# Kernel optimization log

Hardware: AMD Instinct MI355X
Metric: run time of the kernel (lower is better)

The kernel has to match this reference:

```python
import jax, jax.numpy as jnp
import numpy as np

S = 8192  # query length
T = 8192  # key/value length
D = 256   # head dim


def setup_inputs() -> dict:
    key = jax.random.key(0)
    kq, kk, kv = jax.random.split(key, 3)
    return {
        "query": jax.random.normal(kq, (S, D), dtype=jnp.float32),
        "key": jax.random.normal(kk, (T, D), dtype=jnp.float32),
        "value": jax.random.normal(kv, (T, D), dtype=jnp.float32),
    }


def reference(query, key, value):
    # attn_weights = Q @ K^T  (contract last dims, no batch dims)  -> [S, T]
    attn_weights = jnp.einsum("sd,td->st", query, key)
    # SoftmaxAttn: softmax over axes [ndim//2, ndim) == last axis for 2D
    attn_weights = jax.nn.softmax(attn_weights, axis=-1).astype(jnp.float32)
    # y = A @ V  -> [S, D]
    y = jnp.einsum("st,td->sd", attn_weights, value)
    return y
```

## Files before the change

kernel.cpp:

```cpp
#include <hip/hip_runtime.h>
#include <hip/hip_fp16.h>

#define S_LEN 8192
#define T_LEN 8192
#define D_DIM 256
#define QBLK 128
#define KVBLK 32
#define TSPLIT 8
#define NKV ((T_LEN / TSPLIT) / KVBLK)
#define NQT (S_LEN / QBLK)
#define KTILE_BYTES 16384
#define VTILE_BYTES 16384
#define RESCALE_THR 6.0f
#define LOG2E 1.44269504f
#define SMEM_BYTES 81920

typedef _Float16 f16x8 __attribute__((ext_vector_type(8)));
typedef float f32x4 __attribute__((ext_vector_type(4)));

struct h4 { _Float16 h[4]; };

#define GLOAD_LDS16(g, l)                                              \
    __builtin_amdgcn_global_load_lds(                                  \
        (const __attribute__((address_space(1))) void*)(g),            \
        (__attribute__((address_space(3))) void*)(l), 16, 0, 0)

#define MFMA16(a, b, c) __builtin_amdgcn_mfma_f32_16x16x32_f16(a, b, c, 0, 0, 0)

#if __has_builtin(__builtin_amdgcn_exp2f)
#define EXP2(x) __builtin_amdgcn_exp2f(x)
#else
static __device__ __forceinline__ float EXP2(float x) {
    float y;
    asm("v_exp_f32 %0, %1" : "=v"(y) : "v"(x));
    return y;
}
#endif

__global__ __launch_bounds__(256) void cvt_kernel(const float* __restrict__ in,
                                                  _Float16* __restrict__ out, int n4) {
    int i = blockIdx.x * 256 + threadIdx.x;
    if (i < n4) {
        float4 v = ((const float4*)in)[i];
        h4 o;
        o.h[0] = (_Float16)(v.x * LOG2E); o.h[1] = (_Float16)(v.y * LOG2E);
        o.h[2] = (_Float16)(v.z * LOG2E); o.h[3] = (_Float16)(v.w * LOG2E);
        ((h4*)out)[i] = o;
    }
}

__global__ __launch_bounds__(256) void cvt_swz_kernel(const float* __restrict__ in,
                                                      _Float16* __restrict__ img,
                                                      int nchunks) {
    int id = blockIdx.x * 256 + threadIdx.x;
    if (id >= nchunks) return;
    int row = id >> 5, gr = id & 31;
    int t = row >> 5, r = row & 31;
    float4 a = *(const float4*)(in + (size_t)row * D_DIM + gr * 8);
    float4 b = *(const float4*)(in + (size_t)row * D_DIM + gr * 8 + 4);
    f16x8 o;
    o[0] = (_Float16)a.x; o[1] = (_Float16)a.y; o[2] = (_Float16)a.z; o[3] = (_Float16)a.w;
    o[4] = (_Float16)b.x; o[5] = (_Float16)b.y; o[6] = (_Float16)b.z; o[7] = (_Float16)b.w;
    *(f16x8*)((char*)img + (size_t)t * KTILE_BYTES + (gr >> 2) * 2048 +
              ((r >> 4) << 10) + ((r & 15) << 6) + ((gr & 3) << 4)) = o;
}

__global__ __launch_bounds__(256) void vt_swz_kernel(const float* __restrict__ V,
                                                     _Float16* __restrict__ Vimg) {
    __shared__ float tile[32][260];
    const int t = blockIdx.x;
#pragma unroll
    for (int i = 0; i < 8; ++i) {
        int idx = i * 256 + threadIdx.x;
        int kr = idx >> 6, c4 = idx & 63;
        float4 v = *(const float4*)(V + ((size_t)t * 32 + kr) * D_DIM + c4 * 4);
        tile[kr][c4 * 4 + 0] = v.x;
        tile[kr][c4 * 4 + 1] = v.y;
        tile[kr][c4 * 4 + 2] = v.z;
        tile[kr][c4 * 4 + 3] = v.w;
    }
    __syncthreads();
#pragma unroll
    for (int i = 0; i < 4; ++i) {
        int gid = i * 256 + threadIdx.x;
        int d = gid >> 2, gk = gid & 3;
        f16x8 o;
#pragma unroll
        for (int j = 0; j < 8; ++j)
            o[j] = (_Float16)tile[(j >> 2) * 16 + gk * 4 + (j & 3)][d];
        *(f16x8*)((char*)Vimg + (size_t)t * VTILE_BYTES + ((d >> 4) << 10) +
                  (gk << 8) + ((d & 15) << 4)) = o;
    }
}

__global__ __launch_bounds__(256, 2) void attn_kernel(
    const _Float16* __restrict__ Qh, const _Float16* __restrict__ Kimg,
    const _Float16* __restrict__ Vimg, _Float16* __restrict__ Opart,
    float* __restrict__ ml) {
    extern __shared__ __align__(16) char smem[];
    char* sK = smem;
    char* sV = smem + 32768;
    const int tid = threadIdx.x;
    const int wave = tid >> 6, lane = tid & 63;
    const int g = lane >> 4, c = lane & 15;
    const int bid = blockIdx.x;
    const int qtile = bid >> 3, split = bid & 7;
    const int tile0 = split * NKV;
    const int rot = ((qtile >> 5) << 4) | ((qtile & 3) << 2);
    const int othr = tid * 16;
    const int kbase = ((lane & 15) << 6) | ((lane >> 4) << 4);
    const int vbase = lane << 4;

#define TILE_AT(k) (tile0 + (((k) + rot) & (NKV - 1)))
#define STAGE_KV(k, kslot, vslot)                                                  \
    {                                                                              \
        const char* Kt = (const char*)Kimg + (size_t)TILE_AT(k) * KTILE_BYTES;     \
        const char* Vt = (const char*)Vimg + (size_t)TILE_AT(k) * VTILE_BYTES;     \
        _Pragma("unroll") for (int i = 0; i < 4; ++i) {                            \
            GLOAD_LDS16(Kt + i * 4096 + othr, sK + (kslot)*16384 + i * 4096 + othr); \
            GLOAD_LDS16(Vt + i * 4096 + othr, sV + (vslot)*16384 + i * 4096 + othr); \
        }                                                                          \
    }

    f16x8 qf[2][8];
    {
        const size_t qrow0 = (size_t)qtile * QBLK + wave * 32 + c;
#pragma unroll
        for (int mi = 0; mi < 2; ++mi)
#pragma unroll
            for (int ks = 0; ks < 8; ++ks)
                qf[mi][ks] =
                    *(const f16x8*)(Qh + (qrow0 + mi * 16) * D_DIM + (ks * 4 + g) * 8);
    }
    asm volatile("s_waitcnt vmcnt(0)" ::: "memory");

    f32x4 acc[2][16];
#pragma unroll
    for (int mi = 0; mi < 2; ++mi)
#pragma unroll
        for (int dt = 0; dt < 16; ++dt) acc[mi][dt] = (f32x4){0.f, 0.f, 0.f, 0.f};
    float m[2] = {-1e30f, -1e30f};
    float l[2] = {0.f, 0.f};

    STAGE_KV(0, 0, 0);
    STAGE_KV(1, 1, 1);
    asm volatile("s_waitcnt vmcnt(8)" ::: "memory");
    __builtin_amdgcn_s_barrier();

    f32x4 st[2][2];
#pragma unroll
    for (int mi = 0; mi < 2; ++mi)
#pragma unroll
        for (int ct = 0; ct < 2; ++ct) st[mi][ct] = (f32x4){0.f, 0.f, 0.f, 0.f};
    __builtin_amdgcn_s_setprio(1);
#pragma unroll
    for (int ks = 0; ks < 8; ++ks) {
        f16x8 kf0 = *(const f16x8*)(sK + ks * 2048 + kbase);
        f16x8 kf1 = *(const f16x8*)(sK + ks * 2048 + 1024 + kbase);
        st[0][0] = MFMA16(kf0, qf[0][ks], st[0][0]);
        st[0][1] = MFMA16(kf1, qf[0][ks], st[0][1]);
        st[1][0] = MFMA16(kf0, qf[1][ks], st[1][0]);
        st[1][1] = MFMA16(kf1, qf[1][ks], st[1][1]);
    }
    __builtin_amdgcn_s_setprio(0);
    __builtin_amdgcn_s_barrier();

    for (int kt = 0; kt < NKV; ++kt) {
        if (kt + 2 < NKV) {
            STAGE_KV(kt + 2, kt & 1, (kt + 2) % 3);
            asm volatile("s_waitcnt vmcnt(8)" ::: "memory");
        } else {
            asm volatile("s_waitcnt vmcnt(0)" ::: "memory");
        }
        __builtin_amdgcn_s_barrier();

        f32x4 stn[2][2];
#pragma unroll
        for (int mi = 0; mi < 2; ++mi)
#pragma unroll
            for (int ct = 0; ct < 2; ++ct) stn[mi][ct] = (f32x4){0.f, 0.f, 0.f, 0.f};
        if (kt + 1 < NKV) {
            const char* sKb = sK + ((kt + 1) & 1) * 16384;
            __builtin_amdgcn_s_setprio(1);
#pragma unroll
            for (int ks = 0; ks < 8; ++ks) {
                f16x8 kf0 = *(const f16x8*)(sKb + ks * 2048 + kbase);
                f16x8 kf1 = *(const f16x8*)(sKb + ks * 2048 + 1024 + kbase);
                stn[0][0] = MFMA16(kf0, qf[0][ks], stn[0][0]);
                stn[0][1] = MFMA16(kf1, qf[0][ks], stn[0][1]);
                stn[1][0] = MFMA16(kf0, qf[1][ks], stn[1][0]);
                stn[1][1] = MFMA16(kf1, qf[1][ks], stn[1][1]);
            }
            __builtin_amdgcn_s_setprio(0);
        }

        union PU { unsigned int u[4]; f16x8 v; };
        PU pu[2];
#pragma unroll
        for (int mi = 0; mi < 2; ++mi) {
            float pm = fmaxf(fmaxf(fmaxf(st[mi][0][0], st[mi][0][1]),
                                   fmaxf(st[mi][0][2], st[mi][0][3])),
                             fmaxf(fmaxf(st[mi][1][0], st[mi][1][1]),
                                   fmaxf(st[mi][1][2], st[mi][1][3])));
            if (__any(pm > m[mi] + RESCALE_THR)) {
                pm = fmaxf(pm, __shfl_xor(pm, 16));
                pm = fmaxf(pm, __shfl_xor(pm, 32));
                float mn = fmaxf(m[mi], pm);
                float sc = EXP2(m[mi] - mn);
                m[mi] = mn;
                l[mi] *= sc;
                float fr[4];
#pragma unroll
                for (int r = 0; r < 4; ++r) fr[r] = __shfl(sc, (g << 4) | (g * 4 + r));
#pragma unroll
                for (int dt = 0; dt < 16; ++dt)
#pragma unroll
                    for (int r = 0; r < 4; ++r) acc[mi][dt][r] *= fr[r];
            }
            float rs = 0.f;
#pragma unroll
            for (int ct = 0; ct < 2; ++ct)
#pragma unroll
                for (int r = 0; r < 4; ++r) {
                    float p = EXP2(st[mi][ct][r] - m[mi]);
                    st[mi][ct][r] = p;
                    rs += p;
                }
            l[mi] += rs;
            pu[mi].u[0] = __builtin_bit_cast(
                unsigned int, __builtin_amdgcn_cvt_pkrtz(st[mi][0][0], st[mi][0][1]));
            pu[mi].u[1] = __builtin_bit_cast(
                unsigned int, __builtin_amdgcn_cvt_pkrtz(st[mi][0][2], st[mi][0][3]));
            pu[mi].u[2] = __builtin_bit_cast(
                unsigned int, __builtin_amdgcn_cvt_pkrtz(st[mi][1][0], st[mi][1][1]));
            pu[mi].u[3] = __builtin_bit_cast(
                unsigned int, __builtin_amdgcn_cvt_pkrtz(st[mi][1][2], st[mi][1][3]));
        }

        {
            const char* sVb = sV + (kt % 3) * 16384;
            __builtin_amdgcn_s_setprio(1);
#pragma unroll
            for (int dt = 0; dt < 16; ++dt) {
                f16x8 vf = *(const f16x8*)(sVb + dt * 1024 + vbase);
                acc[0][dt] = MFMA16(pu[0].v, vf, acc[0][dt]);
                acc[1][dt] = MFMA16(pu[1].v, vf, acc[1][dt]);
            }
            __builtin_amdgcn_s_setprio(0);
        }

#pragma unroll
        for (int mi = 0; mi < 2; ++mi)
#pragma unroll
            for (int ct = 0; ct < 2; ++ct) st[mi][ct] = stn[mi][ct];

        __builtin_amdgcn_s_barrier();
    }

    _Float16* Ob = Opart + (size_t)(qtile * TSPLIT + split) * QBLK * D_DIM;
#pragma unroll
    for (int mi = 0; mi < 2; ++mi)
#pragma unroll
        for (int dt = 0; dt < 16; ++dt)
#pragma unroll
            for (int r = 0; r < 4; ++r) {
                int row = wave * 32 + mi * 16 + g * 4 + r;
                int col = dt * 16 + c;
                Ob[(size_t)row * D_DIM + col] = (_Float16)acc[mi][dt][r];
            }
#pragma unroll
    for (int mi = 0; mi < 2; ++mi) {
        l[mi] += __shfl_xor(l[mi], 16);
        l[mi] += __shfl_xor(l[mi], 32);
    }
    if (g == 0) {
        float* mlb = ml + (size_t)((qtile * TSPLIT + split) * QBLK) * 2;
#pragma unroll
        for (int mi = 0; mi < 2; ++mi) {
            int row = wave * 32 + mi * 16 + c;
            mlb[row * 2 + 0] = m[mi];
            mlb[row * 2 + 1] = l[mi];
        }
    }
}

__global__ __launch_bounds__(256) void combine_kernel(const _Float16* __restrict__ Opart,
                                                      const float* __restrict__ ml,
                                                      float* __restrict__ out) {
    int r = blockIdx.x;
    int qtile = r >> 7, rl = r & 127;
    int d = threadIdx.x;
    float mv[TSPLIT], lv[TSPLIT];
    float M = -1e30f;
#pragma unroll
    for (int s = 0; s < TSPLIT; ++s) {
        const float* mlb = ml + (size_t)((qtile * TSPLIT + s) * QBLK + rl) * 2;
        mv[s] = mlb[0];
        lv[s] = mlb[1];
        M = fmaxf(M, mv[s]);
    }
    float num = 0.f, den = 0.f;
#pragma unroll
    for (int s = 0; s < TSPLIT; ++s) {
        float w = EXP2(mv[s] - M);
        num += w * (float)Opart[((size_t)(qtile * TSPLIT + s) * QBLK + rl) * D_DIM + d];
        den += w * lv[s];
    }
    out[(size_t)r * D_DIM + d] = num / den;
}

extern "C" void kernel_launch(void* const* d_in, const int* in_sizes, int n_in,
                              void* d_out, int out_size, void* d_ws, size_t ws_size,
                              hipStream_t stream) {
    const float* Q = (const float*)d_in[0];
    const float* K = (const float*)d_in[1];
    const float* V = (const float*)d_in[2];
    float* out = (float*)d_out;
    char* ws = (char*)d_ws;

    _Float16* Qh = (_Float16*)ws;
    _Float16* Kimg = (_Float16*)(ws + (4 << 20));
    _Float16* Vimg = (_Float16*)(ws + (8 << 20));
    _Float16* Opart = (_Float16*)(ws + (12 << 20));
    float* ml = (float*)(ws + ((size_t)44 << 20));

    const int n4 = S_LEN * D_DIM / 4;
    const int nchunks = S_LEN * D_DIM / 8;
    cvt_kernel<<<n4 / 256, 256, 0, stream>>>(Q, Qh, n4);
    cvt_swz_kernel<<<nchunks / 256, 256, 0, stream>>>(K, Kimg, nchunks);
    vt_swz_kernel<<<T_LEN / 32, 256, 0, stream>>>(V, Vimg);

    attn_kernel<<<NQT * TSPLIT, 256, SMEM_BYTES, stream>>>(Qh, Kimg, Vimg, Opart, ml);
    combine_kernel<<<S_LEN, 256, 0, stream>>>(Opart, ml, out);
}
```

Before: 107.6 us.

## Replace software-pipelined QK prefetch with simple double-buffered KV loop

Drops the three-slot V ring and the one-tile-ahead QK^T computation, and uses plain double buffering: wait for all loads, barrier, issue the next tile's K/V loads, then compute QK^T, softmax and PV for the current tile. Shared memory shrinks from 80KB to 64KB, which may allow more resident blocks per CU. The cost is less overlap between loads and compute, since every iteration fully drains vmcnt before proceeding. There is also a single barrier per iteration instead of two.

```diff
diff --git a/kernel.cpp b/kernel.cpp
--- a/kernel.cpp
+++ b/kernel.cpp
@@ -13,7 +13,7 @@
 #define VTILE_BYTES 16384
 #define RESCALE_THR 6.0f
 #define LOG2E 1.44269504f
-#define SMEM_BYTES 81920
+#define SMEM_BYTES 65536
 
 typedef _Float16 f16x8 __attribute__((ext_vector_type(8)));
 typedef float f32x4 __attribute__((ext_vector_type(4)));
@@ -112,13 +112,13 @@
     const int vbase = lane << 4;
 
 #define TILE_AT(k) (tile0 + (((k) + rot) & (NKV - 1)))
-#define STAGE_KV(k, kslot, vslot)                                                  \
+#define STAGE_KV(k, slot)                                                          \
     {                                                                              \
         const char* Kt = (const char*)Kimg + (size_t)TILE_AT(k) * KTILE_BYTES;     \
         const char* Vt = (const char*)Vimg + (size_t)TILE_AT(k) * VTILE_BYTES;     \
         _Pragma("unroll") for (int i = 0; i < 4; ++i) {                            \
-            GLOAD_LDS16(Kt + i * 4096 + othr, sK + (kslot)*16384 + i * 4096 + othr); \
-            GLOAD_LDS16(Vt + i * 4096 + othr, sV + (vslot)*16384 + i * 4096 + othr); \
+            GLOAD_LDS16(Kt + i * 4096 + othr, sK + (slot)*16384 + i * 4096 + othr); \
+            GLOAD_LDS16(Vt + i * 4096 + othr, sV + (slot)*16384 + i * 4096 + othr); \
         }                                                                          \
     }
 
@@ -132,7 +132,6 @@
                 qf[mi][ks] =
                     *(const f16x8*)(Qh + (qrow0 + mi * 16) * D_DIM + (ks * 4 + g) * 8);
     }
-    asm volatile("s_waitcnt vmcnt(0)" ::: "memory");
 
     f32x4 acc[2][16];
 #pragma unroll
@@ -142,57 +141,34 @@
     float m[2] = {-1e30f, -1e30f};
     float l[2] = {0.f, 0.f};
 
-    STAGE_KV(0, 0, 0);
-    STAGE_KV(1, 1, 1);
-    asm volatile("s_waitcnt vmcnt(8)" ::: "memory");
-    __builtin_amdgcn_s_barrier();
-
-    f32x4 st[2][2];
-#pragma unroll
-    for (int mi = 0; mi < 2; ++mi)
-#pragma unroll
-        for (int ct = 0; ct < 2; ++ct) st[mi][ct] = (f32x4){0.f, 0.f, 0.f, 0.f};
-    __builtin_amdgcn_s_setprio(1);
-#pragma unroll
-    for (int ks = 0; ks < 8; ++ks) {
-        f16x8 kf0 = *(const f16x8*)(sK + ks * 2048 + kbase);
-        f16x8 kf1 = *(const f16x8*)(sK + ks * 2048 + 1024 + kbase);
-        st[0][0] = MFMA16(kf0, qf[0][ks], st[0][0]);
-        st[0][1] = MFMA16(kf1, qf[0][ks], st[0][1]);
-        st[1][0] = MFMA16(kf0, qf[1][ks], st[1][0]);
-        st[1][1] = MFMA16(kf1, qf[1][ks], st[1][1]);
-    }
-    __builtin_amdgcn_s_setprio(0);
-    __builtin_amdgcn_s_barrier();
+    STAGE_KV(0, 0);
 
     for (int kt = 0; kt < NKV; ++kt) {
-        if (kt + 2 < NKV) {
-            STAGE_KV(kt + 2, kt & 1, (kt + 2) % 3);
-            asm volatile("s_waitcnt vmcnt(8)" ::: "memory");
-        } else {
-            asm volatile("s_waitcnt vmcnt(0)" ::: "memory");
+        asm volatile("s_waitcnt lgkmcnt(0)" ::: "memory");
+        asm volatile("s_waitcnt vmcnt(0)" ::: "memory");
+        __builtin_amdgcn_s_barrier();
+
+        if (kt + 1 < NKV) STAGE_KV(kt + 1, (kt + 1) & 1);
+
+        const char* sKb = sK + (kt & 1) * 16384;
+        const char* sVb = sV + (kt & 1) * 16384;
+
+        f32x4 st[2][2];
+#pragma unroll
+        for (int mi = 0; mi < 2; ++mi)
+#pragma unroll
+            for (int ct = 0; ct < 2; ++ct) st[mi][ct] = (f32x4){0.f, 0.f, 0.f, 0.f};
+        __builtin_amdgcn_s_setprio(1);
+#pragma unroll
+        for (int ks = 0; ks < 8; ++ks) {
+            f16x8 kf0 = *(const f16x8*)(sKb + ks * 2048 + kbase);
+            f16x8 kf1 = *(const f16x8*)(sKb + ks * 2048 + 1024 + kbase);
+            st[0][0] = MFMA16(kf0, qf[0][ks], st[0][0]);
+            st[0][1] = MFMA16(kf1, qf[0][ks], st[0][1]);
+            st[1][0] = MFMA16(kf0, qf[1][ks], st[1][0]);
+            st[1][1] = MFMA16(kf1, qf[1][ks], st[1][1]);
         }
-        __builtin_amdgcn_s_barrier();
-
-        f32x4 stn[2][2];
-#pragma unroll
-        for (int mi = 0; mi < 2; ++mi)
-#pragma unroll
-            for (int ct = 0; ct < 2; ++ct) stn[mi][ct] = (f32x4){0.f, 0.f, 0.f, 0.f};
-        if (kt + 1 < NKV) {
-            const char* sKb = sK + ((kt + 1) & 1) * 16384;
-            __builtin_amdgcn_s_setprio(1);
-#pragma unroll
-            for (int ks = 0; ks < 8; ++ks) {
-                f16x8 kf0 = *(const f16x8*)(sKb + ks * 2048 + kbase);
-                f16x8 kf1 = *(const f16x8*)(sKb + ks * 2048 + 1024 + kbase);
-                stn[0][0] = MFMA16(kf0, qf[0][ks], stn[0][0]);
-                stn[0][1] = MFMA16(kf1, qf[0][ks], stn[0][1]);
-                stn[1][0] = MFMA16(kf0, qf[1][ks], stn[1][0]);
-                stn[1][1] = MFMA16(kf1, qf[1][ks], stn[1][1]);
-            }
-            __builtin_amdgcn_s_setprio(0);
-        }
+        __builtin_amdgcn_s_setprio(0);
 
         union PU { unsigned int u[4]; f16x8 v; };
         PU pu[2];
@@ -237,24 +213,14 @@
                 unsigned int, __builtin_amdgcn_cvt_pkrtz(st[mi][1][2], st[mi][1][3]));
         }
 
-        {
-            const char* sVb = sV + (kt % 3) * 16384;
-            __builtin_amdgcn_s_setprio(1);
-#pragma unroll
-            for (int dt = 0; dt < 16; ++dt) {
-                f16x8 vf = *(const f16x8*)(sVb + dt * 1024 + vbase);
-                acc[0][dt] = MFMA16(pu[0].v, vf, acc[0][dt]);
-                acc[1][dt] = MFMA16(pu[1].v, vf, acc[1][dt]);
-            }
-            __builtin_amdgcn_s_setprio(0);
+        __builtin_amdgcn_s_setprio(1);
+#pragma unroll
+        for (int dt = 0; dt < 16; ++dt) {
+            f16x8 vf = *(const f16x8*)(sVb + dt * 1024 + vbase);
+            acc[0][dt] = MFMA16(pu[0].v, vf, acc[0][dt]);
+            acc[1][dt] = MFMA16(pu[1].v, vf, acc[1][dt]);
         }
-
-#pragma unroll
-        for (int mi = 0; mi < 2; ++mi)
-#pragma unroll
-            for (int ct = 0; ct < 2; ++ct) st[mi][ct] = stn[mi][ct];
-
-        __builtin_amdgcn_s_barrier();
+        __builtin_amdgcn_s_setprio(0);
     }
 
     _Float16* Ob = Opart + (size_t)(qtile * TSPLIT + split) * QBLK * D_DIM;
```

New measurement: 103.3 us. 4.0% less time.
